# Kernel optimization log

Measured on AMD Instinct MI355X. Metric: run time of the kernel, lower is better.

Reference implementation:

```python
import jax, jax.numpy as jnp
import numpy as np


def setup_inputs() -> dict:
    key = jax.random.key(0)
    ks = jax.random.split(key, 5)
    B, C, H, W = 4, 256, 64, 64
    C8 = C // 8
    x = jax.random.normal(ks[0], (B, C, H, W), dtype=jnp.float32)
    # conv1x1 weights stored as [out, in] (kernel size 1 squeezed)
    wq = jax.random.normal(ks[1], (C8, C), dtype=jnp.float32) * (1.0 / np.sqrt(C))
    wk = jax.random.normal(ks[2], (C8, C), dtype=jnp.float32) * (1.0 / np.sqrt(C))
    wv = jax.random.normal(ks[3], (C, C), dtype=jnp.float32) * (1.0 / np.sqrt(C))
    bq = jnp.zeros((C8,), dtype=jnp.float32)
    bk = jnp.zeros((C8,), dtype=jnp.float32)
    bv = jnp.zeros((C,), dtype=jnp.float32)
    gamma = jax.random.normal(ks[4], (1,), dtype=jnp.float32)
    return {"x": x, "wq": wq, "bq": bq, "wk": wk, "bk": bk, "wv": wv, "bv": bv, "gamma": gamma}


def reference(x, wq, bq, wk, bk, wv, bv, gamma):
    B, C, H, W = x.shape
    flat = x.reshape(B, C, H * W)                      # [B, C, N]
    # 1x1 conv == channel matmul
    q = jnp.einsum('oc,bcn->bon', wq, flat) + bq[:, None]   # [B, C/8, N]
    k = jnp.einsum('oc,bcn->bon', wk, flat) + bk[:, None]   # [B, C/8, N]
    v = jnp.einsum('oc,bcn->bon', wv, flat) + bv[:, None]   # [B, C, N]
    # query permuted to [B, N, C/8]; scores [B, N, N]
    qk = jnp.einsum('bcn,bcm->bnm', q, k)
    # NOTE: softmax over dim=1 (over query index n), matching torch softmax(qk, 1)
    attn = jax.nn.softmax(qk, axis=1)
    out_attn = jnp.einsum('bcn,bnm->bcm', v, attn)     # [B, C, N]
    out = gamma[0] * out_attn.reshape(B, C, H, W) + x
    return out
```

## Files before the change

### kernel.cpp

```cpp
#include <hip/hip_runtime.h>

#define Bsz 4
#define Cch 256
#define Nsp 4096
#define XT_STRIDE 264

typedef _Float16 half8 __attribute__((ext_vector_type(8)));
typedef _Float16 half4v __attribute__((ext_vector_type(4)));
typedef short short8_t __attribute__((ext_vector_type(8)));
typedef float f32x4 __attribute__((ext_vector_type(4)));
typedef float fl4 __attribute__((ext_vector_type(4)));
typedef unsigned short ushort4v __attribute__((ext_vector_type(4)));

static __device__ __forceinline__ unsigned short f2bf(float f) {
  unsigned u = __builtin_bit_cast(unsigned, f);
  u += 0x7FFFu + ((u >> 16) & 1u);
  return (unsigned short)(u >> 16);
}

__global__ __launch_bounds__(256) void wconv_kernel(
    const float* __restrict__ wq, const float* __restrict__ wk, const float* __restrict__ wv,
    const float* __restrict__ bq, const float* __restrict__ bk, const float* __restrict__ bv,
    _Float16* __restrict__ Wh, float* __restrict__ bias)
{
  int t = blockIdx.x * 256 + threadIdx.x;
  int idx0 = t * 4;
  int o = idx0 >> 8, c = idx0 & 255;
  const float* src = (o < 32) ? (wq + o * 256)
                   : (o < 64) ? (wk + (o - 32) * 256)
                              : (wv + (o - 64) * 256);
  fl4 w4 = *(const fl4*)(src + c);
  half4v h;
#pragma unroll
  for (int j = 0; j < 4; ++j) h[j] = (_Float16)w4[j];
  *(half4v*)(Wh + idx0) = h;
  if (t < 320) bias[t] = (t < 32) ? bq[t] : (t < 64) ? bk[t - 32] : bv[t - 64];
}

__global__ __launch_bounds__(256) void proj_kernel(
    const float* __restrict__ x, const _Float16* __restrict__ Wh,
    const float* __restrict__ bias,
    _Float16* __restrict__ qh, _Float16* __restrict__ kh,
    unsigned short* __restrict__ vbuf)
{
  int bid = blockIdx.x;
  int nt  = bid & 127;
  int b   = bid >> 7;
  int n0  = nt * 32;
  int tid = threadIdx.x;
  int w   = tid >> 6, lane = tid & 63;
  int l15 = lane & 15, lg = lane >> 4;

  __shared__ __align__(16) _Float16 xT[32 * XT_STRIDE];

  const float* xb = x + (size_t)b * Cch * Nsp;

  {
    int n = lane & 31, ch = lane >> 5;
#pragma unroll
    for (int i = 0; i < 4; ++i) {
      int c0 = i * 64 + w * 16 + ch * 8;
      half8 hv;
#pragma unroll
      for (int j = 0; j < 8; ++j)
        hv[j] = (_Float16)xb[(size_t)(c0 + j) * Nsp + n0 + n];
      *(half8*)&xT[n * XT_STRIDE + c0] = hv;
    }
  }
  __syncthreads();

  int nsub = (w & 1) * 16;
  half8 bX[8];
#pragma unroll
  for (int k = 0; k < 8; ++k)
    bX[k] = *(const half8*)&xT[(nsub + l15) * XT_STRIDE + k * 32 + lg * 8];

  int n = n0 + nsub + l15;
  int ot0 = (w >> 1) * 10;
#pragma unroll
  for (int t = 0; t < 10; ++t) {
    int ot = ot0 + t;
    const _Float16* wrow = Wh + (size_t)(ot * 16 + l15) * 256 + lg * 8;
    f32x4 acc; acc[0]=0.f; acc[1]=0.f; acc[2]=0.f; acc[3]=0.f;
#pragma unroll
    for (int k = 0; k < 8; ++k) {
      half8 aW = *(const half8*)(wrow + k * 32);
      acc = __builtin_amdgcn_mfma_f32_16x16x32_f16(aW, bX[k], acc, 0, 0, 0);
    }
    fl4 bs = *(const fl4*)(bias + ot * 16 + lg * 4);
    if (ot < 2) {
      half4v qv;
#pragma unroll
      for (int r = 0; r < 4; ++r) qv[r] = (_Float16)(acc[r] + bs[r]);
      *(half4v*)(qh + ((size_t)b * Nsp + n) * 32 + ot * 16 + lg * 4) = qv;
    } else if (ot < 4) {
      half4v kv;
#pragma unroll
      for (int r = 0; r < 4; ++r) kv[r] = (_Float16)(acc[r] + bs[r]);
      *(half4v*)(kh + ((size_t)b * Nsp + n) * 32 + (ot - 2) * 16 + lg * 4) = kv;
    } else {
      int cv = (ot - 4) * 16 + lg * 4;
#pragma unroll
      for (int r = 0; r < 4; ++r)
        vbuf[((size_t)b * Cch + cv + r) * Nsp + n] = f2bf(acc[r] + bs[r]);
    }
  }
}

__global__ __launch_bounds__(512) void attn_kernel(
    const _Float16* __restrict__ qh, const _Float16* __restrict__ kh,
    const unsigned short* __restrict__ vb, const float* __restrict__ x,
    const float* __restrict__ gamma, float* __restrict__ out)
{
  int bid  = blockIdx.x;
  int xcd  = bid & 7;
  int slot = bid >> 3;
  int b    = xcd >> 1;
  int mt   = slot + 32 * (xcd & 1);
  int m0   = mt * 64;
  int tid  = threadIdx.x;
  int w    = tid >> 6;
  int lane = tid & 63;
  int l15  = lane & 15, lg = lane >> 4;

  __shared__ __align__(16) unsigned short P_lds[64][136];
  __shared__ float dpart[8][64];
  __shared__ float denom_s[64];

  const _Float16*       qb    = qh + (size_t)b * Nsp * 32;
  const _Float16*       kb    = kh + (size_t)b * Nsp * 32;
  const unsigned short* vbase = vb + (size_t)b * Cch * Nsp;

  half8 kB[4];
#pragma unroll
  for (int j = 0; j < 4; ++j)
    kB[j] = *(const half8*)(kb + (size_t)(m0 + 16 * j + l15) * 32 + lg * 8);

  f32x4 acc[2][4];
#pragma unroll
  for (int i = 0; i < 2; ++i)
#pragma unroll
    for (int j = 0; j < 4; ++j) { acc[i][j][0]=0.f; acc[i][j][1]=0.f; acc[i][j][2]=0.f; acc[i][j][3]=0.f; }

  float dsum[4] = {0.f, 0.f, 0.f, 0.f};

  for (int n0 = 0; n0 < Nsp; n0 += 128) {
    half8 qA = *(const half8*)(qb + (size_t)(n0 + 16 * w + l15) * 32 + lg * 8);
    f32x4 S[4];
#pragma unroll
    for (int j = 0; j < 4; ++j) {
      f32x4 z; z[0]=0.f; z[1]=0.f; z[2]=0.f; z[3]=0.f;
      S[j] = __builtin_amdgcn_mfma_f32_16x16x32_f16(qA, kB[j], z, 0, 0, 0);
    }
    ushort4v pb[4];
#pragma unroll
    for (int j = 0; j < 4; ++j) {
#pragma unroll
      for (int r = 0; r < 4; ++r) {
        float p = __expf(S[j][r] - 20.0f);
        dsum[j] += p;
        pb[j][r] = f2bf(p);
      }
    }
    __syncthreads();
#pragma unroll
    for (int j = 0; j < 4; ++j)
      *(ushort4v*)&P_lds[16 * j + l15][16 * w + lg * 4] = pb[j];
    __syncthreads();
    __builtin_amdgcn_s_setprio(1);
#pragma unroll
    for (int k = 0; k < 4; ++k) {
      short8_t bP[4];
#pragma unroll
      for (int j = 0; j < 4; ++j)
        bP[j] = *(const short8_t*)&P_lds[16 * j + l15][k * 32 + lg * 8];
#pragma unroll
      for (int c16 = 0; c16 < 2; ++c16) {
        short8_t aV = *(const short8_t*)(vbase + (size_t)(32 * w + 16 * c16 + l15) * Nsp
                                         + n0 + k * 32 + lg * 8);
#pragma unroll
        for (int j = 0; j < 4; ++j)
          acc[c16][j] = __builtin_amdgcn_mfma_f32_16x16x32_bf16(aV, bP[j], acc[c16][j], 0, 0, 0);
      }
    }
    __builtin_amdgcn_s_setprio(0);
  }

#pragma unroll
  for (int j = 0; j < 4; ++j) {
    float d = dsum[j];
    d += __shfl_xor(d, 16);
    d += __shfl_xor(d, 32);
    dsum[j] = d;
  }
  if (lane < 16) {
#pragma unroll
    for (int j = 0; j < 4; ++j) dpart[w][16 * j + lane] = dsum[j];
  }
  __syncthreads();
  if (tid < 64) {
    float s = 0.f;
#pragma unroll
    for (int ww = 0; ww < 8; ++ww) s += dpart[ww][tid];
    denom_s[tid] = s;
  }
  __syncthreads();

  float g = gamma[0];
#pragma unroll
  for (int c16 = 0; c16 < 2; ++c16) {
#pragma unroll
    for (int j = 0; j < 4; ++j) {
      float dn = denom_s[16 * j + l15];
#pragma unroll
      for (int r = 0; r < 4; ++r) {
        int c = 32 * w + 16 * c16 + lg * 4 + r;
        int m = m0 + 16 * j + l15;
        size_t idx = ((size_t)b * Cch + c) * Nsp + m;
        out[idx] = g * (acc[c16][j][r] / dn) + x[idx];
      }
    }
  }
}

extern "C" void kernel_launch(void* const* d_in, const int* in_sizes, int n_in,
                              void* d_out, int out_size, void* d_ws, size_t ws_size,
                              hipStream_t stream) {
  const float* x     = (const float*)d_in[0];
  const float* wq    = (const float*)d_in[1];
  const float* bq    = (const float*)d_in[2];
  const float* wk    = (const float*)d_in[3];
  const float* bk    = (const float*)d_in[4];
  const float* wv    = (const float*)d_in[5];
  const float* bv    = (const float*)d_in[6];
  const float* gamma = (const float*)d_in[7];
  float* out = (float*)d_out;

  char* ws = (char*)d_ws;
  _Float16*       qh   = (_Float16*)ws;
  _Float16*       kh   = (_Float16*)(ws + (1u << 20));
  unsigned short* vb   = (unsigned short*)(ws + (2u << 20));
  _Float16*       Wh   = (_Float16*)(ws + (10u << 20));
  float*          bias = (float*)(ws + (10u << 20) + (320u * 256u * 2u));

  wconv_kernel<<<dim3(80), dim3(256), 0, stream>>>(wq, wk, wv, bq, bk, bv, Wh, bias);
  proj_kernel<<<dim3(512), dim3(256), 0, stream>>>(x, Wh, bias, qh, kh, vb);
  attn_kernel<<<dim3(256), dim3(512), 0, stream>>>(qh, kh, vb, x, gamma, out);
}
```

Baseline: 133.9 us.

## Retile attention PV GEMM across warps, double-buffer and swizzle P in LDS

The PV GEMM warp tiling moves from 32 channels x 64 queries per warp to 64 channels x 32 queries. This halves the P fragments each warp reads from LDS, but each V fragment is now loaded by two warps. V fragments for the whole 128-wide chunk are prefetched into registers before the QK/softmax step, which overlaps global loads with compute. P is double-buffered with an XOR swizzle, so one barrier per iteration is dropped and LDS bank conflicts are reduced. The cost is higher register pressure (16 V fragments), with launch_bounds set to 1 block per CU.

```diff
diff --git a/kernel.cpp b/kernel.cpp
--- a/kernel.cpp
+++ b/kernel.cpp
@@ -107,7 +107,7 @@
   }
 }
 
-__global__ __launch_bounds__(512) void attn_kernel(
+__global__ __launch_bounds__(512, 1) void attn_kernel(
     const _Float16* __restrict__ qh, const _Float16* __restrict__ kh,
     const unsigned short* __restrict__ vb, const float* __restrict__ x,
     const float* __restrict__ gamma, float* __restrict__ out)
@@ -122,8 +122,9 @@
   int w    = tid >> 6;
   int lane = tid & 63;
   int l15  = lane & 15, lg = lane >> 4;
-
-  __shared__ __align__(16) unsigned short P_lds[64][136];
+  int wm   = w >> 2, wc = w & 3;
+
+  __shared__ __align__(16) unsigned short P_lds[2][64][128];
   __shared__ float dpart[8][64];
   __shared__ float denom_s[64];
 
@@ -136,16 +137,25 @@
   for (int j = 0; j < 4; ++j)
     kB[j] = *(const half8*)(kb + (size_t)(m0 + 16 * j + l15) * 32 + lg * 8);
 
-  f32x4 acc[2][4];
-#pragma unroll
-  for (int i = 0; i < 2; ++i)
-#pragma unroll
-    for (int j = 0; j < 4; ++j) { acc[i][j][0]=0.f; acc[i][j][1]=0.f; acc[i][j][2]=0.f; acc[i][j][3]=0.f; }
+  f32x4 acc[4][2];
+#pragma unroll
+  for (int i = 0; i < 4; ++i)
+#pragma unroll
+    for (int j = 0; j < 2; ++j) { acc[i][j][0]=0.f; acc[i][j][1]=0.f; acc[i][j][2]=0.f; acc[i][j][3]=0.f; }
 
   float dsum[4] = {0.f, 0.f, 0.f, 0.f};
 
   for (int n0 = 0; n0 < Nsp; n0 += 128) {
+    int buf = (n0 >> 7) & 1;
     half8 qA = *(const half8*)(qb + (size_t)(n0 + 16 * w + l15) * 32 + lg * 8);
+    short8_t vfrag[4][4];
+#pragma unroll
+    for (int k = 0; k < 4; ++k)
+#pragma unroll
+      for (int c16 = 0; c16 < 4; ++c16)
+        vfrag[k][c16] = *(const short8_t*)(vbase
+            + (size_t)(64 * wc + 16 * c16 + l15) * Nsp + n0 + k * 32 + lg * 8);
+
     f32x4 S[4];
 #pragma unroll
     for (int j = 0; j < 4; ++j) {
@@ -162,26 +172,28 @@
         pb[j][r] = f2bf(p);
       }
     }
-    __syncthreads();
-#pragma unroll
-    for (int j = 0; j < 4; ++j)
-      *(ushort4v*)&P_lds[16 * j + l15][16 * w + lg * 4] = pb[j];
+#pragma unroll
+    for (int j = 0; j < 4; ++j) {
+      int prow = 16 * j + l15;
+      int pcol = (16 * w + lg * 4) ^ ((prow & 7) << 3);
+      *(ushort4v*)&P_lds[buf][prow][pcol] = pb[j];
+    }
     __syncthreads();
     __builtin_amdgcn_s_setprio(1);
 #pragma unroll
     for (int k = 0; k < 4; ++k) {
-      short8_t bP[4];
-#pragma unroll
-      for (int j = 0; j < 4; ++j)
-        bP[j] = *(const short8_t*)&P_lds[16 * j + l15][k * 32 + lg * 8];
-#pragma unroll
-      for (int c16 = 0; c16 < 2; ++c16) {
-        short8_t aV = *(const short8_t*)(vbase + (size_t)(32 * w + 16 * c16 + l15) * Nsp
-                                         + n0 + k * 32 + lg * 8);
-#pragma unroll
-        for (int j = 0; j < 4; ++j)
-          acc[c16][j] = __builtin_amdgcn_mfma_f32_16x16x32_bf16(aV, bP[j], acc[c16][j], 0, 0, 0);
+      short8_t bP[2];
+#pragma unroll
+      for (int jj = 0; jj < 2; ++jj) {
+        int prow = 16 * (2 * wm + jj) + l15;
+        int pcol = (k * 32 + lg * 8) ^ ((prow & 7) << 3);
+        bP[jj] = *(const short8_t*)&P_lds[buf][prow][pcol];
       }
+#pragma unroll
+      for (int c16 = 0; c16 < 4; ++c16)
+#pragma unroll
+        for (int jj = 0; jj < 2; ++jj)
+          acc[c16][jj] = __builtin_amdgcn_mfma_f32_16x16x32_bf16(vfrag[k][c16], bP[jj], acc[c16][jj], 0, 0, 0);
     }
     __builtin_amdgcn_s_setprio(0);
   }
@@ -208,16 +220,16 @@
 
   float g = gamma[0];
 #pragma unroll
-  for (int c16 = 0; c16 < 2; ++c16) {
-#pragma unroll
-    for (int j = 0; j < 4; ++j) {
-      float dn = denom_s[16 * j + l15];
+  for (int c16 = 0; c16 < 4; ++c16) {
+#pragma unroll
+    for (int jj = 0; jj < 2; ++jj) {
+      float dn = denom_s[16 * (2 * wm + jj) + l15];
 #pragma unroll
       for (int r = 0; r < 4; ++r) {
-        int c = 32 * w + 16 * c16 + lg * 4 + r;
-        int m = m0 + 16 * j + l15;
+        int c = 64 * wc + 16 * c16 + lg * 4 + r;
+        int m = m0 + 16 * (2 * wm + jj) + l15;
         size_t idx = ((size_t)b * Cch + c) * Nsp + m;
-        out[idx] = g * (acc[c16][j][r] / dn) + x[idx];
+        out[idx] = g * (acc[c16][jj][r] / dn) + x[idx];
       }
     }
   }
```

After: 153.9 us. 15.0% more time.

## Split attention K-dimension across two wave groups with double-buffered swizzled P tile

Applied to the files above, without the earlier changes.

The attention kernel now runs 1024 threads per block. Sixteen waves each compute scores for 16 query rows per iteration, covering 256 rows at a time. The two groups of eight waves each accumulate P·V over half of that chunk, and their partial accumulators are summed through LDS at the end. The P tile is double-buffered with an XOR swizzle, which removes one barrier per iteration and reduces LDS bank conflicts. The cost is a larger LDS footprint, higher register pressure under the 1024-thread launch bound, and an extra reduction step.

```diff
diff --git a/kernel.cpp b/kernel.cpp
--- a/kernel.cpp
+++ b/kernel.cpp
@@ -107,7 +107,7 @@
   }
 }
 
-__global__ __launch_bounds__(512) void attn_kernel(
+__global__ __launch_bounds__(1024) void attn_kernel(
     const _Float16* __restrict__ qh, const _Float16* __restrict__ kh,
     const unsigned short* __restrict__ vb, const float* __restrict__ x,
     const float* __restrict__ gamma, float* __restrict__ out)
@@ -122,9 +122,10 @@
   int w    = tid >> 6;
   int lane = tid & 63;
   int l15  = lane & 15, lg = lane >> 4;
-
-  __shared__ __align__(16) unsigned short P_lds[64][136];
-  __shared__ float dpart[8][64];
+  int wk   = w >> 3, wc = w & 7;
+
+  __shared__ __align__(16) unsigned short P_lds[2][64][256];
+  __shared__ float dpart[16][64];
   __shared__ float denom_s[64];
 
   const _Float16*       qb    = qh + (size_t)b * Nsp * 32;
@@ -144,8 +145,16 @@
 
   float dsum[4] = {0.f, 0.f, 0.f, 0.f};
 
-  for (int n0 = 0; n0 < Nsp; n0 += 128) {
-    half8 qA = *(const half8*)(qb + (size_t)(n0 + 16 * w + l15) * 32 + lg * 8);
+  const _Float16*       qp  = qb + (size_t)(16 * w + l15) * 32 + lg * 8;
+  const unsigned short* pv0 = vbase + (size_t)(32 * wc + l15) * Nsp + 128 * wk + lg * 8;
+  const unsigned short* pv1 = pv0 + (size_t)16 * Nsp;
+  int xorh  = 8 * (l15 & 7);
+  int wcol  = (16 * w + 4 * lg) ^ xorh;
+  int rbase = 128 * wk + 8 * lg;
+
+  for (int it = 0; it < 16; ++it) {
+    int buf = it & 1;
+    half8 qA = *(const half8*)qp;  qp += 256 * 32;
     f32x4 S[4];
 #pragma unroll
     for (int j = 0; j < 4; ++j) {
@@ -162,28 +171,28 @@
         pb[j][r] = f2bf(p);
       }
     }
+#pragma unroll
+    for (int j = 0; j < 4; ++j)
+      *(ushort4v*)&P_lds[buf][16 * j + l15][wcol] = pb[j];
     __syncthreads();
-#pragma unroll
-    for (int j = 0; j < 4; ++j)
-      *(ushort4v*)&P_lds[16 * j + l15][16 * w + lg * 4] = pb[j];
-    __syncthreads();
+    const unsigned short* pk0 = pv0;
+    const unsigned short* pk1 = pv1;
     __builtin_amdgcn_s_setprio(1);
 #pragma unroll
     for (int k = 0; k < 4; ++k) {
-      short8_t bP[4];
-#pragma unroll
-      for (int j = 0; j < 4; ++j)
-        bP[j] = *(const short8_t*)&P_lds[16 * j + l15][k * 32 + lg * 8];
-#pragma unroll
-      for (int c16 = 0; c16 < 2; ++c16) {
-        short8_t aV = *(const short8_t*)(vbase + (size_t)(32 * w + 16 * c16 + l15) * Nsp
-                                         + n0 + k * 32 + lg * 8);
-#pragma unroll
-        for (int j = 0; j < 4; ++j)
-          acc[c16][j] = __builtin_amdgcn_mfma_f32_16x16x32_bf16(aV, bP[j], acc[c16][j], 0, 0, 0);
+      short8_t aV0 = *(const short8_t*)pk0;
+      short8_t aV1 = *(const short8_t*)pk1;
+      pk0 += 32; pk1 += 32;
+#pragma unroll
+      for (int j = 0; j < 4; ++j) {
+        int rc = (rbase + 32 * k) ^ xorh;
+        short8_t bP = *(const short8_t*)&P_lds[buf][16 * j + l15][rc];
+        acc[0][j] = __builtin_amdgcn_mfma_f32_16x16x32_bf16(aV0, bP, acc[0][j], 0, 0, 0);
+        acc[1][j] = __builtin_amdgcn_mfma_f32_16x16x32_bf16(aV1, bP, acc[1][j], 0, 0, 0);
       }
     }
     __builtin_amdgcn_s_setprio(0);
+    pv0 += 256; pv1 += 256;
   }
 
 #pragma unroll
@@ -201,23 +210,35 @@
   if (tid < 64) {
     float s = 0.f;
 #pragma unroll
-    for (int ww = 0; ww < 8; ++ww) s += dpart[ww][tid];
+    for (int ww = 0; ww < 16; ++ww) s += dpart[ww][tid];
     denom_s[tid] = s;
   }
+  float* mbuf = (float*)P_lds;
+  if (w >= 8) {
+#pragma unroll
+    for (int c16 = 0; c16 < 2; ++c16)
+#pragma unroll
+      for (int j = 0; j < 4; ++j)
+#pragma unroll
+        for (int r = 0; r < 4; ++r)
+          mbuf[lane + 64 * (((c16 * 4 + j) * 4 + r) + 32 * (w - 8))] = acc[c16][j][r];
+  }
   __syncthreads();
-
-  float g = gamma[0];
-#pragma unroll
-  for (int c16 = 0; c16 < 2; ++c16) {
-#pragma unroll
-    for (int j = 0; j < 4; ++j) {
-      float dn = denom_s[16 * j + l15];
-#pragma unroll
-      for (int r = 0; r < 4; ++r) {
-        int c = 32 * w + 16 * c16 + lg * 4 + r;
-        int m = m0 + 16 * j + l15;
-        size_t idx = ((size_t)b * Cch + c) * Nsp + m;
-        out[idx] = g * (acc[c16][j][r] / dn) + x[idx];
+  if (w < 8) {
+    float g = gamma[0];
+#pragma unroll
+    for (int c16 = 0; c16 < 2; ++c16) {
+#pragma unroll
+      for (int j = 0; j < 4; ++j) {
+        float dn = denom_s[16 * j + l15];
+#pragma unroll
+        for (int r = 0; r < 4; ++r) {
+          float a = acc[c16][j][r] + mbuf[lane + 64 * (((c16 * 4 + j) * 4 + r) + 32 * w)];
+          int c = 32 * w + 16 * c16 + 4 * lg + r;
+          int m = m0 + 16 * j + l15;
+          size_t idx = ((size_t)b * Cch + c) * Nsp + m;
+          out[idx] = g * (a / dn) + x[idx];
+        }
       }
     }
   }
@@ -245,5 +266,5 @@
 
   wconv_kernel<<<dim3(80), dim3(256), 0, stream>>>(wq, wk, wv, bq, bk, bv, Wh, bias);
   proj_kernel<<<dim3(512), dim3(256), 0, stream>>>(x, Wh, bias, qh, kh, vb);
-  attn_kernel<<<dim3(256), dim3(512), 0, stream>>>(qh, kh, vb, x, gamma, out);
-}
+  attn_kernel<<<dim3(256), dim3(1024), 0, stream>>>(qh, kh, vb, x, gamma, out);
+}
```

Result: faster. 114.1 us (-14.7%).

## Halve attention m-tile, double grid, double-buffer P in LDS, prefetch V

Applied to the files above, without the earlier changes.

The attention kernel now covers 32 key columns per block instead of 64 and launches 512 blocks instead of 256, giving more blocks per CU for occupancy. P is double-buffered in LDS, which removes one barrier per iteration. V fragments are loaded into registers at the top of each iteration, before the QK MFMA, so they are in flight during it. exp is rewritten as exp2 with a fused multiply-add. The trade-off is that each block reads the full V stream for only half the columns, doubling V traffic from L2.

```diff
diff --git a/kernel.cpp b/kernel.cpp
--- a/kernel.cpp
+++ b/kernel.cpp
@@ -4,6 +4,7 @@
 #define Cch 256
 #define Nsp 4096
 #define XT_STRIDE 264
+#define PST 136
 
 typedef _Float16 half8 __attribute__((ext_vector_type(8)));
 typedef _Float16 half4v __attribute__((ext_vector_type(4)));
@@ -11,6 +12,9 @@
 typedef float f32x4 __attribute__((ext_vector_type(4)));
 typedef float fl4 __attribute__((ext_vector_type(4)));
 typedef unsigned short ushort4v __attribute__((ext_vector_type(4)));
+
+#define LOG2E 1.4426950408889634f
+#define NSHIFT (-28.853900817779268f)
 
 static __device__ __forceinline__ unsigned short f2bf(float f) {
   unsigned u = __builtin_bit_cast(unsigned, f);
@@ -114,80 +118,85 @@
 {
   int bid  = blockIdx.x;
   int xcd  = bid & 7;
-  int slot = bid >> 3;
+  int s    = bid >> 3;
   int b    = xcd >> 1;
-  int mt   = slot + 32 * (xcd & 1);
-  int m0   = mt * 64;
+  int m0   = 32 * (s + 64 * (xcd & 1));
   int tid  = threadIdx.x;
   int w    = tid >> 6;
   int lane = tid & 63;
   int l15  = lane & 15, lg = lane >> 4;
 
-  __shared__ __align__(16) unsigned short P_lds[64][136];
-  __shared__ float dpart[8][64];
-  __shared__ float denom_s[64];
+  __shared__ __align__(16) unsigned short P_lds[2][32][PST];
+  __shared__ float dpart[8][32];
+  __shared__ float denom_s[32];
 
   const _Float16*       qb    = qh + (size_t)b * Nsp * 32;
   const _Float16*       kb    = kh + (size_t)b * Nsp * 32;
   const unsigned short* vbase = vb + (size_t)b * Cch * Nsp;
 
-  half8 kB[4];
-#pragma unroll
-  for (int j = 0; j < 4; ++j)
+  half8 kB[2];
+#pragma unroll
+  for (int j = 0; j < 2; ++j)
     kB[j] = *(const half8*)(kb + (size_t)(m0 + 16 * j + l15) * 32 + lg * 8);
 
-  f32x4 acc[2][4];
+  f32x4 acc[2][2];
 #pragma unroll
   for (int i = 0; i < 2; ++i)
 #pragma unroll
-    for (int j = 0; j < 4; ++j) { acc[i][j][0]=0.f; acc[i][j][1]=0.f; acc[i][j][2]=0.f; acc[i][j][3]=0.f; }
-
-  float dsum[4] = {0.f, 0.f, 0.f, 0.f};
-
-  for (int n0 = 0; n0 < Nsp; n0 += 128) {
-    half8 qA = *(const half8*)(qb + (size_t)(n0 + 16 * w + l15) * 32 + lg * 8);
-    f32x4 S[4];
-#pragma unroll
-    for (int j = 0; j < 4; ++j) {
+    for (int j = 0; j < 2; ++j) { acc[i][j][0]=0.f; acc[i][j][1]=0.f; acc[i][j][2]=0.f; acc[i][j][3]=0.f; }
+
+  float dsum[2] = {0.f, 0.f};
+
+  const _Float16*       qp  = qb + (size_t)(16 * w + l15) * 32 + lg * 8;
+  const unsigned short* pv0 = vbase + (size_t)(32 * w + l15) * Nsp + lg * 8;
+  const unsigned short* pv1 = pv0 + (size_t)16 * Nsp;
+  int wcol = 16 * w + 4 * lg;
+
+  for (int it = 0; it < 32; ++it) {
+    int buf = it & 1;
+    half8 qA = *(const half8*)qp;  qp += 128 * 32;
+    short8_t vf[4][2];
+#pragma unroll
+    for (int k = 0; k < 4; ++k) {
+      vf[k][0] = *(const short8_t*)(pv0 + 32 * k);
+      vf[k][1] = *(const short8_t*)(pv1 + 32 * k);
+    }
+    pv0 += 128; pv1 += 128;
+    f32x4 S[2];
+#pragma unroll
+    for (int j = 0; j < 2; ++j) {
       f32x4 z; z[0]=0.f; z[1]=0.f; z[2]=0.f; z[3]=0.f;
       S[j] = __builtin_amdgcn_mfma_f32_16x16x32_f16(qA, kB[j], z, 0, 0, 0);
     }
-    ushort4v pb[4];
-#pragma unroll
-    for (int j = 0; j < 4; ++j) {
+    ushort4v pb[2];
+#pragma unroll
+    for (int j = 0; j < 2; ++j) {
 #pragma unroll
       for (int r = 0; r < 4; ++r) {
-        float p = __expf(S[j][r] - 20.0f);
+        float p = exp2f(fmaf(S[j][r], LOG2E, NSHIFT));
         dsum[j] += p;
         pb[j][r] = f2bf(p);
       }
     }
-    __syncthreads();
-#pragma unroll
-    for (int j = 0; j < 4; ++j)
-      *(ushort4v*)&P_lds[16 * j + l15][16 * w + lg * 4] = pb[j];
+#pragma unroll
+    for (int j = 0; j < 2; ++j)
+      *(ushort4v*)&P_lds[buf][16 * j + l15][wcol] = pb[j];
     __syncthreads();
     __builtin_amdgcn_s_setprio(1);
 #pragma unroll
     for (int k = 0; k < 4; ++k) {
-      short8_t bP[4];
-#pragma unroll
-      for (int j = 0; j < 4; ++j)
-        bP[j] = *(const short8_t*)&P_lds[16 * j + l15][k * 32 + lg * 8];
-#pragma unroll
-      for (int c16 = 0; c16 < 2; ++c16) {
-        short8_t aV = *(const short8_t*)(vbase + (size_t)(32 * w + 16 * c16 + l15) * Nsp
-                                         + n0 + k * 32 + lg * 8);
-#pragma unroll
-        for (int j = 0; j < 4; ++j)
-          acc[c16][j] = __builtin_amdgcn_mfma_f32_16x16x32_bf16(aV, bP[j], acc[c16][j], 0, 0, 0);
-      }
+      short8_t bP0 = *(const short8_t*)&P_lds[buf][l15][32 * k + 8 * lg];
+      short8_t bP1 = *(const short8_t*)&P_lds[buf][16 + l15][32 * k + 8 * lg];
+      acc[0][0] = __builtin_amdgcn_mfma_f32_16x16x32_bf16(vf[k][0], bP0, acc[0][0], 0, 0, 0);
+      acc[0][1] = __builtin_amdgcn_mfma_f32_16x16x32_bf16(vf[k][0], bP1, acc[0][1], 0, 0, 0);
+      acc[1][0] = __builtin_amdgcn_mfma_f32_16x16x32_bf16(vf[k][1], bP0, acc[1][0], 0, 0, 0);
+      acc[1][1] = __builtin_amdgcn_mfma_f32_16x16x32_bf16(vf[k][1], bP1, acc[1][1], 0, 0, 0);
     }
     __builtin_amdgcn_s_setprio(0);
   }
 
 #pragma unroll
-  for (int j = 0; j < 4; ++j) {
+  for (int j = 0; j < 2; ++j) {
     float d = dsum[j];
     d += __shfl_xor(d, 16);
     d += __shfl_xor(d, 32);
@@ -195,14 +204,14 @@
   }
   if (lane < 16) {
 #pragma unroll
-    for (int j = 0; j < 4; ++j) dpart[w][16 * j + lane] = dsum[j];
+    for (int j = 0; j < 2; ++j) dpart[w][16 * j + lane] = dsum[j];
   }
   __syncthreads();
-  if (tid < 64) {
-    float s = 0.f;
-#pragma unroll
-    for (int ww = 0; ww < 8; ++ww) s += dpart[ww][tid];
-    denom_s[tid] = s;
+  if (tid < 32) {
+    float sden = 0.f;
+#pragma unroll
+    for (int ww = 0; ww < 8; ++ww) sden += dpart[ww][tid];
+    denom_s[tid] = sden;
   }
   __syncthreads();
 
@@ -210,11 +219,11 @@
 #pragma unroll
   for (int c16 = 0; c16 < 2; ++c16) {
 #pragma unroll
-    for (int j = 0; j < 4; ++j) {
+    for (int j = 0; j < 2; ++j) {
       float dn = denom_s[16 * j + l15];
 #pragma unroll
       for (int r = 0; r < 4; ++r) {
-        int c = 32 * w + 16 * c16 + lg * 4 + r;
+        int c = 32 * w + 16 * c16 + 4 * lg + r;
         int m = m0 + 16 * j + l15;
         size_t idx = ((size_t)b * Cch + c) * Nsp + m;
         out[idx] = g * (acc[c16][j][r] / dn) + x[idx];
@@ -245,5 +254,5 @@
 
   wconv_kernel<<<dim3(80), dim3(256), 0, stream>>>(wq, wk, wv, bq, bk, bv, Wh, bias);
   proj_kernel<<<dim3(512), dim3(256), 0, stream>>>(x, Wh, bias, qh, kh, vb);
-  attn_kernel<<<dim3(256), dim3(512), 0, stream>>>(qh, kh, vb, x, gamma, out);
-}
+  attn_kernel<<<dim3(512), dim3(512), 0, stream>>>(qh, kh, vb, x, gamma, out);
+}
```

After: 157.9 us. +18.0%, slower.
